# Kernel tuning notes

Hardware: AMD Instinct MI355X
Metric: run time of the kernel (lower is better)

Reference implementation:

```python
import jax, jax.numpy as jnp
import numpy as np

S, B, E, H, O, WL, PL, T = 128, 64, 1024, 1024, 135, 64, 32, 100


def setup_inputs() -> dict:
    key = jax.random.key(0)
    ks = jax.random.split(key, 12)
    rn = lambda k, shape, s=1.0: jax.random.normal(k, shape, jnp.float32) * s
    return dict(
        encoder_states=rn(ks[0], (S, B, E)),
        encoder_hidden=rn(ks[1], (2, B, E // 2)),
        previous_poses=rn(ks[2], (PL, B, O)),
        words=rn(ks[3], (WL, B, 200)),
        real_poses_len=T,
        W_ed=rn(ks[4], (H, E), 0.02), b_ed=jnp.zeros((H,), jnp.float32),
        W_att=rn(ks[5], (H, E), 0.02), b_att=jnp.zeros((H,), jnp.float32),
        W_watt=rn(ks[6], (H, 200), 0.02), b_watt=jnp.zeros((H,), jnp.float32),
        W_ih=rn(ks[7], (3 * H, O), 0.02), W_hh=rn(ks[8], (3 * H, H), 0.02),
        b_ih=jnp.zeros((3 * H,), jnp.float32), b_hh=jnp.zeros((3 * H,), jnp.float32),
        W_out=rn(ks[9], (O, 3 * H), 0.02), b_out=jnp.zeros((O,), jnp.float32),
    )


def _gru_step(x, h, W_ih, W_hh, b_ih, b_hh):
    # PyTorch GRU cell: gates ordered (r, z, n)
    gi = x @ W_ih.T + b_ih  # [B, 3H]
    gh = h @ W_hh.T + b_hh  # [B, 3H]
    Hd = h.shape[-1]
    ir, iz, inn = gi[:, :Hd], gi[:, Hd:2 * Hd], gi[:, 2 * Hd:]
    hr, hz, hn = gh[:, :Hd], gh[:, Hd:2 * Hd], gh[:, 2 * Hd:]
    r = jax.nn.sigmoid(ir + hr)
    z = jax.nn.sigmoid(iz + hz)
    n = jnp.tanh(inn + r * hn)
    return (1.0 - z) * n + z * h


def _attend(proj, h):
    # proj: [S, B, H] (already enc_to_dec-projected), h: [B, H]
    scores = jnp.einsum('sbh,bh->bs', proj, h)
    w = jax.nn.softmax(scores, axis=1)
    return jnp.einsum('sbh,bs->bh', proj, w)  # [B, H]


def reference(encoder_states, encoder_hidden, previous_poses, words, real_poses_len,
              W_ed, b_ed, W_att, b_att, W_watt, b_watt,
              W_ih, W_hh, b_ih, b_hh, W_out, b_out):
    s, b, e = encoder_states.shape
    # take last bidirectional layer, merge directions -> [B, E]
    eh = encoder_hidden.reshape(-1, 2, b, e // 2)[-1]          # [2, B, E/2]
    h = jnp.transpose(eh, (1, 0, 2)).reshape(b, e) @ W_ed.T + b_ed  # [B, H]

    # warm-up GRU pass over previous poses (only final hidden is used)
    def warm(hc, x):
        return _gru_step(x, hc, W_ih, W_hh, b_ih, b_hh), None
    h, _ = jax.lax.scan(warm, h, previous_poses)

    # attention projections are step-invariant: hoist out of the loop
    enc_proj = encoder_states @ W_att.T + b_att   # [S, B, H]
    word_proj = words @ W_watt.T + b_watt         # [WL, B, H]

    start = previous_poses[-1]                    # [B, O]

    def step(carry, _):
        pose, hc = carry
        hc = _gru_step(pose, hc, W_ih, W_hh, b_ih, b_hh)
        ctx = _attend(enc_proj, hc)
        wctx = _attend(word_proj, hc)
        cat = jnp.concatenate([hc, ctx, wctx], axis=1)  # [B, 3H]; dropout = identity (eval)
        pose = cat @ W_out.T + b_out                    # [B, O]
        return (pose, hc), pose

    _, poses = jax.lax.scan(step, (start, h), None, length=real_poses_len)
    return poses  # [T, B, O]
```

## Files before the change

### kernel.cpp

```cpp
#include <hip/hip_runtime.h>
#include <cstdint>
#include <cstddef>

typedef unsigned short ushort_t;
typedef __attribute__((ext_vector_type(8))) short short8;
typedef __attribute__((ext_vector_type(4))) float floatx4;

#define SS 128
#define BB 64
#define EE 1024
#define HH 1024
#define OO 135
#define WLW 64
#define PLP 32
#define TT 100
#define KP 160
#define NWG 64
#define NTH 1024

#define WHH_PITCH 1032
#define WIH_PITCH 168
#define LDS_WHH   0
#define LDS_WIH   99072
#define LDS_CX    115200
#define LDS_SC    127488
#define LDS_WTS   128256
#define LDS_RED   115200
#define RED_GATE  304
#define RED_BT    1216
#define RED_REG   4864

#define FB_DTYPE 0
#define FB_FLAGS 32

static __device__ __forceinline__ float bf2f(ushort_t u) {
    union { unsigned int i; float f; } v; v.i = ((unsigned int)u) << 16; return v.f;
}
static __device__ __forceinline__ ushort_t f2bf(float f) {
    union { float f; unsigned int i; } v; v.f = f;
    unsigned int x = v.i;
    x += 0x7fffu + ((x >> 16) & 1u);
    return (ushort_t)(x >> 16);
}
static __device__ __forceinline__ float ldf(const void* p, long i, unsigned isbf) {
    if (isbf) return bf2f(((const ushort_t*)p)[i]);
    return ((const float*)p)[i];
}
static __device__ __forceinline__ short8 ldfrag(const ushort_t* p) {
    return *reinterpret_cast<const short8*>(p);
}
static __device__ __forceinline__ short8 ldfrag_l(const short* p) {
    return *reinterpret_cast<const short8*>(p);
}
static __device__ __forceinline__ int cxp(int m) {
    return ((m & 15) << 6) | (m >> 4);
}
static __device__ __forceinline__ unsigned long long sysld_u64(const void* p) {
    return __hip_atomic_load((const unsigned long long*)p, __ATOMIC_RELAXED, __HIP_MEMORY_SCOPE_SYSTEM);
}
static __device__ __forceinline__ void sysst_u16(ushort_t* p, ushort_t v) {
    __hip_atomic_store(p, v, __ATOMIC_RELAXED, __HIP_MEMORY_SCOPE_SYSTEM);
}
static __device__ __forceinline__ void sysst_u32(unsigned* p, unsigned v) {
    __hip_atomic_store(p, v, __ATOMIC_RELAXED, __HIP_MEMORY_SCOPE_SYSTEM);
}
static __device__ __forceinline__ unsigned sysld_u32(const unsigned* p) {
    return __hip_atomic_load(p, __ATOMIC_RELAXED, __HIP_MEMORY_SCOPE_SYSTEM);
}
static __device__ __forceinline__ short8 sysld_frag16(const ushort_t* p) {
    union { unsigned long long u[2]; short8 s; } r;
    r.u[0] = sysld_u64(p);
    r.u[1] = sysld_u64(p + 4);
    return r.s;
}
static __device__ __forceinline__ short8 frag_ld(const void* p, unsigned isbf,
                                                 long rowoff, int kbase, int kcap) {
    if (kbase >= kcap) {
        short8 z = {0, 0, 0, 0, 0, 0, 0, 0};
        return z;
    }
    if (isbf) return ldfrag((const ushort_t*)p + rowoff + kbase);
    const float* f = (const float*)p + rowoff + kbase;
    short8 a;
    #pragma unroll
    for (int i = 0; i < 8; ++i) a[i] = (short)f2bf(f[i]);
    return a;
}
static __device__ __forceinline__ floatx4 mfma(short8 a, short8 b, floatx4 c) {
    return __builtin_amdgcn_mfma_f32_16x16x32_bf16(a, b, c, 0, 0, 0);
}
static __device__ __forceinline__ float sigmoidf(float x) {
    x = fminf(fmaxf(x, -30.f), 30.f);
    return 1.f / (1.f + __expf(-x));
}
static __device__ __forceinline__ float tanh_f(float x) {
    x = fminf(fmaxf(x, -15.f), 15.f);
    float e = __expf(2.f * x);
    return (e - 1.f) / (e + 1.f);
}

static __device__ __forceinline__ void gbar(unsigned* flags, unsigned phase) {
    __syncthreads();
    if (threadIdx.x < 64) {
        __builtin_amdgcn_fence(__ATOMIC_RELEASE, "workgroup");
        if (threadIdx.x == 0)
            sysst_u32(&flags[(size_t)blockIdx.x * 32], phase);
        for (;;) {
            unsigned v = sysld_u32(&flags[(size_t)threadIdx.x * 32]);
            if (__all((int)(v >= phase))) break;
            __builtin_amdgcn_s_sleep(1);
        }
        __builtin_amdgcn_fence(__ATOMIC_ACQUIRE, "workgroup");
    }
    __syncthreads();
}

__global__ void k_detect(const unsigned* __restrict__ enc, unsigned* __restrict__ flag)
{
    __shared__ int cnt;
    if (threadIdx.x == 0) cnt = 0;
    __syncthreads();
    unsigned w = enc[threadIdx.x];
    unsigned ef = (w >> 7) & 0xFFu;
    if (ef >= 0x70u && ef <= 0x81u) atomicAdd(&cnt, 1);
    for (int i = threadIdx.x; i < NWG * 32; i += 256)
        sysst_u32(&flag[FB_FLAGS + i], 0u);
    __syncthreads();
    if (threadIdx.x == 0)
        flag[FB_DTYPE] = (cnt >= 200) ? 1u : 0u;
}

__global__ void k_prep(const void* __restrict__ eh, const void* __restrict__ Wih,
                       const void* __restrict__ Wout, const void* __restrict__ pp,
                       const void* __restrict__ Whh,
                       ushort_t* __restrict__ ehcat, ushort_t* __restrict__ wih_p,
                       ushort_t* __restrict__ wout_p, ushort_t* __restrict__ pp_pad,
                       ushort_t* __restrict__ pose_pad, ushort_t* __restrict__ whh_bf,
                       const unsigned* __restrict__ flag)
{
    unsigned isbf = flag[FB_DTYPE];
    long idx = (long)blockIdx.x * 256 + threadIdx.x;
    const long n1 = BB * EE;
    const long n2 = (long)3 * HH * KP;
    const long n3f = (long)144 * 3 * HH;
    const long n4 = (long)PLP * BB * KP;
    const long n5 = (long)BB * KP;
    const long n6 = (long)3 * HH * HH;
    if (idx < n1) {
        int b = (int)(idx >> 10), r = (int)(idx & 1023);
        int c = r >> 9, jj = r & 511;
        ehcat[idx] = f2bf(ldf(eh, (long)(c * BB + b) * 512 + jj, isbf));
        return;
    }
    idx -= n1;
    if (idx < n2) {
        long row = idx / KP, k = idx % KP;
        wih_p[idx] = (k < OO) ? f2bf(ldf(Wih, row * OO + k, isbf)) : (ushort_t)0; return;
    }
    idx -= n2;
    if (idx < n3f) {
        long row = idx / (3 * HH), k = idx % (3 * HH);
        wout_p[idx] = (row < OO) ? f2bf(ldf(Wout, row * (3 * HH) + k, isbf)) : (ushort_t)0; return;
    }
    idx -= n3f;
    if (idx < n4) {
        long t = idx / (BB * KP); long rem = idx % (BB * KP);
        long b = rem / KP, k = rem % KP;
        pp_pad[idx] = (k < OO) ? f2bf(ldf(pp, (t * BB + b) * OO + k, isbf)) : (ushort_t)0; return;
    }
    idx -= n4;
    if (idx < n5) { pose_pad[idx] = 0; return; }
    idx -= n5;
    if (idx < n6) { whh_bf[idx] = f2bf(ldf(Whh, idx, isbf)); return; }
}

__global__ void __launch_bounds__(256) k_gemm(
    const void* __restrict__ A, int a_bf16, int lda, int kcapA,
    const void* __restrict__ B, int b_bf16, int ldb, int kcapB,
    const void* __restrict__ biasRaw,
    float* __restrict__ outF, ushort_t* __restrict__ outB16,
    ushort_t* __restrict__ outHi, ushort_t* __restrict__ outLo,
    int ldo, int M, int N, int K, const unsigned* __restrict__ flag)
{
    unsigned isbf = flag[FB_DTYPE];
    unsigned a_isbf = a_bf16 ? 1u : isbf;
    unsigned b_isbf = b_bf16 ? 1u : isbf;
    int lane = threadIdx.x & 63;
    int wid = (blockIdx.x << 2) + (threadIdx.x >> 6);
    int ng = N >> 6;
    int mt = wid / ng, g = wid % ng;
    if (mt * 16 >= M) return;
    int col = lane & 15, quad = lane >> 4;
    long arow = (long)(mt * 16 + col) * lda;
    long brow0 = (long)((g << 6) + col) * ldb;
    long brow1 = brow0 + (long)16 * ldb;
    long brow2 = brow0 + (long)32 * ldb;
    long brow3 = brow0 + (long)48 * ldb;
    int kb = quad * 8;
    floatx4 ac0 = {0.f, 0.f, 0.f, 0.f}, ac1 = ac0, ac2 = ac0, ac3 = ac0;
    for (int k = 0; k < K; k += 32) {
        short8 av = frag_ld(A, a_isbf, arow, kb + k, kcapA);
        ac0 = mfma(av, frag_ld(B, b_isbf, brow0, kb + k, kcapB), ac0);
        ac1 = mfma(av, frag_ld(B, b_isbf, brow1, kb + k, kcapB), ac1);
        ac2 = mfma(av, frag_ld(B, b_isbf, brow2, kb + k, kcapB), ac2);
        ac3 = mfma(av, frag_ld(B, b_isbf, brow3, kb + k, kcapB), ac3);
    }
    int m0 = mt * 16 + quad * 4;
    #pragma unroll
    for (int tIdx = 0; tIdx < 4; ++tIdx) {
        floatx4 ac = (tIdx == 0) ? ac0 : (tIdx == 1) ? ac1 : (tIdx == 2) ? ac2 : ac3;
        int n = (g << 6) + tIdx * 16 + col;
        float bv = biasRaw ? ldf(biasRaw, n, isbf) : 0.f;
        #pragma unroll
        for (int r = 0; r < 4; ++r) {
            float v = ac[r] + bv;
            size_t o = (size_t)(m0 + r) * ldo + n;
            if (outF) outF[o] = v;
            if (outB16) outB16[o] = f2bf(v);
            if (outHi) {
                ushort_t hi = f2bf(v);
                outHi[o] = hi;
                outLo[o] = f2bf(v - bf2f(hi));
            }
        }
    }
}

__global__ void __launch_bounds__(1024, 4) k_persist(
    const ushort_t* __restrict__ encP,
    const ushort_t* __restrict__ wordP,
    const ushort_t* __restrict__ whh_bf, const ushort_t* __restrict__ wih_p,
    const void* __restrict__ b_ih, const void* __restrict__ b_hh,
    const ushort_t* __restrict__ wout_p,
    const void* __restrict__ b_out,
    const ushort_t* __restrict__ pp_pad, ushort_t* __restrict__ pose_pad,
    float* hFa, float* hFb, ushort_t* hhia, ushort_t* hhib,
    ushort_t* hloa, ushort_t* hlob,
    void* __restrict__ out, unsigned* flagbar)
{
    extern __shared__ char smem[];
    short* whh_lds = (short*)(smem + LDS_WHH);
    short* wih_lds = (short*)(smem + LDS_WIH);
    float* cx  = (float*)(smem + LDS_CX);
    float* sc  = (float*)(smem + LDS_SC);
    float* wts = (float*)(smem + LDS_WTS);
    float* red = (float*)(smem + LDS_RED);

    const int tid = threadIdx.x;
    const int lane = tid & 63, wv = tid >> 6;
    const int wg = blockIdx.x;
    const int col = lane & 15, quad = lane >> 4;
    const int bt = wv & 3;
    const int ks = wv >> 2;
    unsigned isbf = flagbar[FB_DTYPE];
    unsigned* flags = flagbar + FB_FLAGS;
    unsigned bphase = 0;

    float* hFs = hFa; float* hFd = hFb;
    ushort_t* hhis = hhia; ushort_t* hhid = hhib;
    ushort_t* hlos = hloa; ushort_t* hlod = hlob;

    for (int s = tid; s < 48 * 128; s += NTH) {
        int r = s >> 7;
        int ko = (s & 127) << 3;
        int g = r >> 4, rr = r & 15;
        *(short8*)(whh_lds + r * WHH_PITCH + ko) =
            ldfrag(whh_bf + (size_t)g * HH * HH + (size_t)(wg * 16 + rr) * HH + ko);
    }
    for (int s = tid; s < 48 * 20; s += NTH) {
        int r = s / 20;
        int ko = (s % 20) << 3;
        int g = r >> 4, rr = r & 15;
        *(short8*)(wih_lds + r * WIH_PITCH + ko) =
            ldfrag(wih_p + (size_t)g * HH * KP + (size_t)(wg * 16 + rr) * KP + ko);
    }
    __syncthreads();

    const int j = wg * 16 + col;
    const float bir = ldf(b_ih, j, isbf)          + ldf(b_hh, j, isbf);
    const float biz = ldf(b_ih, HH + j, isbf)     + ldf(b_hh, HH + j, isbf);
    const float bin = ldf(b_ih, 2 * HH + j, isbf);
    const float bhn = ldf(b_hh, 2 * HH + j, isbf);

    for (int t = 0; t < PLP + TT; ++t) {
        const bool dec = (t >= PLP);
        const bool warm_src = (t <= PLP);
        const ushort_t* poseA = (t < PLP)  ? (pp_pad + (size_t)t * BB * KP)
                              : (t == PLP) ? (pp_pad + (size_t)(PLP - 1) * BB * KP)
                                           : pose_pad;
        {
            const ushort_t* ah = hhis + (size_t)(bt * 16 + col) * HH + quad * 8;
            const ushort_t* al = hlos + (size_t)(bt * 16 + col) * HH + quad * 8;
            const short* w0 = whh_lds + (size_t)(0  + col) * WHH_PITCH + quad * 8;
            const short* w1 = whh_lds + (size_t)(16 + col) * WHH_PITCH + quad * 8;
            const short* w2 = whh_lds + (size_t)(32 + col) * WHH_PITCH + quad * 8;
            floatx4 aR = {0.f, 0.f, 0.f, 0.f}, aZ = aR, aNi = aR, aNh = aR;
            const int k0 = ks * 256, k1 = k0 + 256;
            #pragma unroll 4
            for (int k = k0; k < k1; k += 32) {
                short8 f0 = ldfrag_l(w0 + k), f1 = ldfrag_l(w1 + k), f2 = ldfrag_l(w2 + k);
                short8 xh = sysld_frag16(ah + k), xl = sysld_frag16(al + k);
                aR = mfma(xh, f0, aR);   aR = mfma(xl, f0, aR);
                aZ = mfma(xh, f1, aZ);   aZ = mfma(xl, f1, aZ);
                aNh = mfma(xh, f2, aNh); aNh = mfma(xl, f2, aNh);
            }
            const ushort_t* ap = poseA + (size_t)(bt * 16 + col) * KP + quad * 8;
            const short* c0 = wih_lds + (size_t)(0  + col) * WIH_PITCH + quad * 8;
            const short* c1 = wih_lds + (size_t)(16 + col) * WIH_PITCH + quad * 8;
            const short* c2 = wih_lds + (size_t)(32 + col) * WIH_PITCH + quad * 8;
            for (int k5 = ks; k5 < 5; k5 += 4) {
                int k = k5 * 32;
                short8 xp = warm_src ? ldfrag(ap + k) : sysld_frag16(ap + k);
                aR = mfma(xp, ldfrag_l(c0 + k), aR);
                aZ = mfma(xp, ldfrag_l(c1 + k), aZ);
                aNi = mfma(xp, ldfrag_l(c2 + k), aNi);
            }
            if (ks == 1 || ks == 3) {
                float* dst = red + (ks >> 1) * RED_REG + bt * RED_BT;
                #pragma unroll
                for (int r = 0; r < 4; ++r) {
                    int idx = (quad * 4 + r) * 19 + col;
                    dst[idx] = aR[r];                  dst[RED_GATE + idx] = aZ[r];
                    dst[2 * RED_GATE + idx] = aNh[r];  dst[3 * RED_GATE + idx] = aNi[r];
                }
            }
            __syncthreads();
            if (ks == 0 || ks == 2) {
                const float* sp = red + (ks >> 1) * RED_REG + bt * RED_BT;
                #pragma unroll
                for (int r = 0; r < 4; ++r) {
                    int idx = (quad * 4 + r) * 19 + col;
                    aR[r] += sp[idx];                  aZ[r] += sp[RED_GATE + idx];
                    aNh[r] += sp[2 * RED_GATE + idx];  aNi[r] += sp[3 * RED_GATE + idx];
                }
            }
            __syncthreads();
            if (ks == 2) {
                float* dst = red + bt * RED_BT;
                #pragma unroll
                for (int r = 0; r < 4; ++r) {
                    int idx = (quad * 4 + r) * 19 + col;
                    dst[idx] = aR[r];                  dst[RED_GATE + idx] = aZ[r];
                    dst[2 * RED_GATE + idx] = aNh[r];  dst[3 * RED_GATE + idx] = aNi[r];
                }
            }
            __syncthreads();
            if (ks == 0) {
                const float* sp = red + bt * RED_BT;
                #pragma unroll
                for (int r = 0; r < 4; ++r) {
                    int idx = (quad * 4 + r) * 19 + col;
                    aR[r] += sp[idx];                  aZ[r] += sp[RED_GATE + idx];
                    aNh[r] += sp[2 * RED_GATE + idx];  aNi[r] += sp[3 * RED_GATE + idx];
                }
                #pragma unroll
                for (int r = 0; r < 4; ++r) {
                    int b = bt * 16 + quad * 4 + r;
                    float hold = hFs[(size_t)b * HH + j];
                    float rg = sigmoidf(aR[r] + bir);
                    float zg = sigmoidf(aZ[r] + biz);
                    float ng = tanh_f(aNi[r] + bin + rg * (aNh[r] + bhn));
                    float hn = (1.f - zg) * ng + zg * hold;
                    hFd[(size_t)b * HH + j] = hn;
                    ushort_t hi = f2bf(hn);
                    sysst_u16(&hhid[(size_t)b * HH + j], hi);
                    sysst_u16(&hlod[(size_t)b * HH + j], f2bf(hn - bf2f(hi)));
                }
            }
        }
        { float* tf = hFs; hFs = hFd; hFd = tf; }
        { ushort_t* tp = hhis; hhis = hhid; hhid = tp;
          tp = hlos; hlos = hlod; hlod = tp; }
        ++bphase;
        gbar(flags, bphase);
        if (!dec) continue;

        {
            const int b = wg;
            if (tid < 256) {
                union { unsigned long long u; ushort_t e[4]; } h4, l4;
                h4.u = sysld_u64(hhis + (size_t)b * HH + tid * 4);
                l4.u = sysld_u64(hlos + (size_t)b * HH + tid * 4);
                #pragma unroll
                for (int i = 0; i < 4; ++i)
                    cx[cxp(tid * 4 + i)] = bf2f(h4.e[i]) + bf2f(l4.e[i]);
            }
            __syncthreads();
            float hreg[16];
            #pragma unroll
            for (int i = 0; i < 16; ++i) hreg[i] = cx[(i << 6) | lane];
            for (int idx = wv; idx < 192; idx += 16) {
                const ushort_t* rp = (idx < 128)
                    ? (encP + ((size_t)(idx * BB + b) << 10))
                    : (wordP + ((size_t)((idx - 128) * BB + b) << 10));
                short8 v0 = ldfrag(rp + lane * 16);
                short8 v1 = ldfrag(rp + lane * 16 + 8);
                float s = 0.f;
                #pragma unroll
                for (int i = 0; i < 8; ++i) s += bf2f((ushort_t)v0[i]) * hreg[i];
                #pragma unroll
                for (int i = 0; i < 8; ++i) s += bf2f((ushort_t)v1[i]) * hreg[8 + i];
                #pragma unroll
                for (int m = 1; m < 64; m <<= 1) s += __shfl_xor(s, m);
                if (lane == 0) sc[idx] = s;
            }
            __syncthreads();
            if (wv == 0) {
                float a = sc[lane], c = sc[lane + 64];
                float mx = fmaxf(a, c);
                #pragma unroll
                for (int m = 1; m < 64; m <<= 1) mx = fmaxf(mx, __shfl_xor(mx, m));
                float e0 = __expf(a - mx), e1 = __expf(c - mx);
                float sm = e0 + e1;
                #pragma unroll
                for (int m = 1; m < 64; m <<= 1) sm += __shfl_xor(sm, m);
                float inv = 1.f / sm;
                wts[lane] = e0 * inv; wts[lane + 64] = e1 * inv;
            } else if (wv == 1) {
                float a = sc[128 + lane];
                float mx = a;
                #pragma unroll
                for (int m = 1; m < 64; m <<= 1) mx = fmaxf(mx, __shfl_xor(mx, m));
                float e0 = __expf(a - mx);
                float sm = e0;
                #pragma unroll
                for (int m = 1; m < 64; m <<= 1) sm += __shfl_xor(sm, m);
                wts[128 + lane] = e0 / sm;
            }
            __syncthreads();
            if (tid < 256) {
                float a0 = 0.f, a1 = 0.f, a2 = 0.f, a3 = 0.f;
                const ushort_t* basep = encP + ((size_t)b << 10) + tid * 4;
                #pragma unroll 8
                for (int s = 0; s < SS; ++s) {
                    float w = wts[s];
                    union { unsigned long long u; ushort_t e[4]; } v;
                    v.u = *(const unsigned long long*)(basep + ((size_t)(s * BB) << 10));
                    a0 += w * bf2f(v.e[0]); a1 += w * bf2f(v.e[1]);
                    a2 += w * bf2f(v.e[2]); a3 += w * bf2f(v.e[3]);
                }
                cx[1024 + cxp(tid * 4 + 0)] = a0; cx[1024 + cxp(tid * 4 + 1)] = a1;
                cx[1024 + cxp(tid * 4 + 2)] = a2; cx[1024 + cxp(tid * 4 + 3)] = a3;
            } else if (tid < 512) {
                int tt = tid - 256;
                float a0 = 0.f, a1 = 0.f, a2 = 0.f, a3 = 0.f;
                const ushort_t* basep = wordP + ((size_t)b << 10) + tt * 4;
                #pragma unroll 8
                for (int s = 0; s < WLW; ++s) {
                    float w = wts[128 + s];
                    union { unsigned long long u; ushort_t e[4]; } v;
                    v.u = *(const unsigned long long*)(basep + ((size_t)(s * BB) << 10));
                    a0 += w * bf2f(v.e[0]); a1 += w * bf2f(v.e[1]);
                    a2 += w * bf2f(v.e[2]); a3 += w * bf2f(v.e[3]);
                }
                cx[2048 + cxp(tt * 4 + 0)] = a0; cx[2048 + cxp(tt * 4 + 1)] = a1;
                cx[2048 + cxp(tt * 4 + 2)] = a2; cx[2048 + cxp(tt * 4 + 3)] = a3;
            }
            __syncthreads();
            float cr[48];
            #pragma unroll
            for (int c3 = 0; c3 < 3; ++c3)
                #pragma unroll
                for (int i = 0; i < 16; ++i)
                    cr[c3 * 16 + i] = cx[c3 * 1024 + (i << 6) + lane];
            int td = t - PLP;
            for (int oo = 0; oo < 9; ++oo) {
                int o = wv * 9 + oo;
                const ushort_t* wr = wout_p + (size_t)o * (3 * HH) + lane * 16;
                float s = 0.f;
                #pragma unroll
                for (int c3 = 0; c3 < 3; ++c3) {
                    short8 w8a = ldfrag(wr + c3 * 1024);
                    short8 w8b = ldfrag(wr + c3 * 1024 + 8);
                    #pragma unroll
                    for (int i = 0; i < 8; ++i) s += bf2f((ushort_t)w8a[i]) * cr[c3 * 16 + i];
                    #pragma unroll
                    for (int i = 0; i < 8; ++i) s += bf2f((ushort_t)w8b[i]) * cr[c3 * 16 + 8 + i];
                }
                #pragma unroll
                for (int m = 1; m < 64; m <<= 1) s += __shfl_xor(s, m);
                if (lane == 0) {
                    float v = s + ((o < OO) ? ldf(b_out, o, isbf) : 0.f);
                    if (o < OO) {
                        size_t oi = ((size_t)td * BB + b) * OO + o;
                        if (isbf) ((ushort_t*)out)[oi] = f2bf(v);
                        else      ((float*)out)[oi] = v;
                    }
                    sysst_u16(&pose_pad[(size_t)b * KP + o], (o < OO) ? f2bf(v) : (ushort_t)0);
                }
            }
        }
        ++bphase;
        gbar(flags, bphase);
    }
}

extern "C" void kernel_launch(void* const* d_in, const int* in_sizes, int n_in,
                              void* d_out, int out_size, void* d_ws, size_t ws_size,
                              hipStream_t stream)
{
    (void)in_sizes; (void)n_in; (void)out_size; (void)ws_size;
    const void* enc_states = d_in[0];
    const void* enc_hidden = d_in[1];
    const void* prev_poses = d_in[2];
    const void* words      = d_in[3];
    const void* W_ed  = d_in[5];
    const void* b_ed  = d_in[6];
    const void* W_att = d_in[7];
    const void* b_att = d_in[8];
    const void* W_watt = d_in[9];
    const void* b_watt = d_in[10];
    const void* W_ih  = d_in[11];
    const void* W_hh  = d_in[12];
    const void* b_ih  = d_in[13];
    const void* b_hh  = d_in[14];
    const void* W_out = d_in[15];
    const void* b_out = d_in[16];

    char* base = (char*)d_ws;
    size_t off = 0;
    auto alloc = [&](size_t bytes) -> char* {
        char* p = base + off;
        off = (off + bytes + 255) & ~(size_t)255;
        return p;
    };
    unsigned* flagbar  = (unsigned*)alloc(128 + (size_t)NWG * 128);
    ushort_t* ehcat    = (ushort_t*)alloc((size_t)BB * EE * 2);
    ushort_t* wih_p    = (ushort_t*)alloc((size_t)3 * HH * KP * 2);
    ushort_t* wout_p   = (ushort_t*)alloc((size_t)144 * 3 * HH * 2);
    ushort_t* pp_pad   = (ushort_t*)alloc((size_t)PLP * BB * KP * 2);
    ushort_t* pose_pad = (ushort_t*)alloc((size_t)BB * KP * 2);
    ushort_t* whh_bf   = (ushort_t*)alloc((size_t)3 * HH * HH * 2);
    float*    hF0      = (float*)alloc((size_t)BB * HH * 4);
    float*    hF1      = (float*)alloc((size_t)BB * HH * 4);
    ushort_t* hhi0     = (ushort_t*)alloc((size_t)BB * HH * 2);
    ushort_t* hhi1     = (ushort_t*)alloc((size_t)BB * HH * 2);
    ushort_t* hlo0     = (ushort_t*)alloc((size_t)BB * HH * 2);
    ushort_t* hlo1     = (ushort_t*)alloc((size_t)BB * HH * 2);
    ushort_t* encP     = (ushort_t*)alloc((size_t)SS * BB * HH * 2);
    ushort_t* wordP    = (ushort_t*)alloc((size_t)WLW * BB * HH * 2);

    k_detect<<<1, 256, 0, stream>>>((const unsigned*)enc_states, flagbar);

    k_prep<<<17512, 256, 0, stream>>>(enc_hidden, W_ih, W_out, prev_poses, W_hh,
                                      ehcat, wih_p, wout_p, pp_pad, pose_pad, whh_bf,
                                      flagbar);

    k_gemm<<<16, 256, 0, stream>>>(ehcat, 1, EE, EE, W_ed, 0, EE, EE, b_ed,
                                   hF0, nullptr, hhi0, hlo0, HH, BB, HH, EE, flagbar);
    k_gemm<<<2048, 256, 0, stream>>>(enc_states, 0, EE, EE, W_att, 0, EE, EE, b_att,
                                     nullptr, encP, nullptr, nullptr, HH, SS * BB, HH, EE, flagbar);
    k_gemm<<<1024, 256, 0, stream>>>(words, 0, 200, 200, W_watt, 0, 200, 200, b_watt,
                                     nullptr, wordP, nullptr, nullptr, HH, WLW * BB, HH, 224, flagbar);

    (void)hipFuncSetAttribute((const void*)k_persist,
                              hipFuncAttributeMaxDynamicSharedMemorySize, 154112);
    k_persist<<<NWG, NTH, 154112, stream>>>(encP, wordP, whh_bf, wih_p,
                                            b_ih, b_hh, wout_p, b_out, pp_pad, pose_pad,
                                            hF0, hF1, hhi0, hhi1, hlo0, hlo1,
                                            d_out, flagbar);
}
```

Measured before the change: 6.171 ms.

## Overlap next-step recurrent matmul with grid barrier and split attention reductions

The grid barrier is split into separate arrive and wait phases. During decode steps, the next step's h·W_hh MFMA partial products run between the two phases, so they overlap with waiting on other workgroups. The four-way cross-wave gate reduction now uses LDS atomicAdd into a single buffer, which is zeroed after use, replacing the two-stage store/sync tree. The context weighted sums are spread across twice as many threads, with a partial-sum combine, and the score loop treats encP and wordP as one contiguous row array. The gains depend on h already being complete at the early call point, and on the two projection buffers being allocated back to back.

Measured after the change: 8.825 ms. 43.0% more time.

```diff
diff --git a/kernel.cpp b/kernel.cpp
--- a/kernel.cpp
+++ b/kernel.cpp
@@ -25,10 +25,11 @@
 #define LDS_CX    115200
 #define LDS_SC    127488
 #define LDS_WTS   128256
-#define LDS_RED   115200
+#define LDS_PART  129024
+#define LDS_RED   137216
 #define RED_GATE  304
 #define RED_BT    1216
-#define RED_REG   4864
+#define SMEM_SZ   156672
 
 #define FB_DTYPE 0
 #define FB_FLAGS 32
@@ -99,12 +100,15 @@
     return (e - 1.f) / (e + 1.f);
 }
 
-static __device__ __forceinline__ void gbar(unsigned* flags, unsigned phase) {
+static __device__ __forceinline__ void g_arrive(unsigned* flags, unsigned phase) {
     __syncthreads();
+    if (threadIdx.x == 0) {
+        __builtin_amdgcn_fence(__ATOMIC_RELEASE, "workgroup");
+        sysst_u32(&flags[(size_t)blockIdx.x * 32], phase);
+    }
+}
+static __device__ __forceinline__ void g_wait(unsigned* flags, unsigned phase) {
     if (threadIdx.x < 64) {
-        __builtin_amdgcn_fence(__ATOMIC_RELEASE, "workgroup");
-        if (threadIdx.x == 0)
-            sysst_u32(&flags[(size_t)blockIdx.x * 32], phase);
         for (;;) {
             unsigned v = sysld_u32(&flags[(size_t)threadIdx.x * 32]);
             if (__all((int)(v >= phase))) break;
@@ -113,6 +117,10 @@
         __builtin_amdgcn_fence(__ATOMIC_ACQUIRE, "workgroup");
     }
     __syncthreads();
+}
+static __device__ __forceinline__ void gbar(unsigned* flags, unsigned phase) {
+    g_arrive(flags, phase);
+    g_wait(flags, phase);
 }
 
 __global__ void k_detect(const unsigned* __restrict__ enc, unsigned* __restrict__ flag)
@@ -227,8 +235,8 @@
 }
 
 __global__ void __launch_bounds__(1024, 4) k_persist(
-    const ushort_t* __restrict__ encP,
-    const ushort_t* __restrict__ wordP,
+    const ushort_t* encP,
+    const ushort_t* wordP,
     const ushort_t* __restrict__ whh_bf, const ushort_t* __restrict__ wih_p,
     const void* __restrict__ b_ih, const void* __restrict__ b_hh,
     const ushort_t* __restrict__ wout_p,
@@ -241,10 +249,11 @@
     extern __shared__ char smem[];
     short* whh_lds = (short*)(smem + LDS_WHH);
     short* wih_lds = (short*)(smem + LDS_WIH);
-    float* cx  = (float*)(smem + LDS_CX);
-    float* sc  = (float*)(smem + LDS_SC);
-    float* wts = (float*)(smem + LDS_WTS);
-    float* red = (float*)(smem + LDS_RED);
+    float* cx   = (float*)(smem + LDS_CX);
+    float* sc   = (float*)(smem + LDS_SC);
+    float* wts  = (float*)(smem + LDS_WTS);
+    float* part = (float*)(smem + LDS_PART);
+    float* red  = (float*)(smem + LDS_RED);
 
     const int tid = threadIdx.x;
     const int lane = tid & 63, wv = tid >> 6;
@@ -274,6 +283,7 @@
         *(short8*)(wih_lds + r * WIH_PITCH + ko) =
             ldfrag(wih_p + (size_t)g * HH * KP + (size_t)(wg * 16 + rr) * KP + ko);
     }
+    for (int i = tid; i < 4 * RED_BT; i += NTH) red[i] = 0.f;
     __syncthreads();
 
     const int j = wg * 16 + col;
@@ -281,6 +291,29 @@
     const float biz = ldf(b_ih, HH + j, isbf)     + ldf(b_hh, HH + j, isbf);
     const float bin = ldf(b_ih, 2 * HH + j, isbf);
     const float bhn = ldf(b_hh, 2 * HH + j, isbf);
+
+    const short* w0 = whh_lds + (size_t)(0  + col) * WHH_PITCH + quad * 8;
+    const short* w1 = whh_lds + (size_t)(16 + col) * WHH_PITCH + quad * 8;
+    const short* w2 = whh_lds + (size_t)(32 + col) * WHH_PITCH + quad * 8;
+    const short* c0 = wih_lds + (size_t)(0  + col) * WIH_PITCH + quad * 8;
+    const short* c1 = wih_lds + (size_t)(16 + col) * WIH_PITCH + quad * 8;
+    const short* c2 = wih_lds + (size_t)(32 + col) * WIH_PITCH + quad * 8;
+    const int k0 = ks * 256, k1 = k0 + 256;
+
+    floatx4 pR = {0.f, 0.f, 0.f, 0.f}, pZ = pR, pNh = pR;
+
+    auto part1 = [&]() {
+        const ushort_t* ah = hhis + (size_t)(bt * 16 + col) * HH + quad * 8;
+        const ushort_t* al = hlos + (size_t)(bt * 16 + col) * HH + quad * 8;
+        #pragma unroll 4
+        for (int k = k0; k < k1; k += 32) {
+            short8 f0 = ldfrag_l(w0 + k), f1 = ldfrag_l(w1 + k), f2 = ldfrag_l(w2 + k);
+            short8 xh = sysld_frag16(ah + k), xl = sysld_frag16(al + k);
+            pR = mfma(xh, f0, pR);   pR = mfma(xl, f0, pR);
+            pZ = mfma(xh, f1, pZ);   pZ = mfma(xl, f1, pZ);
+            pNh = mfma(xh, f2, pNh); pNh = mfma(xl, f2, pNh);
+        }
+    };
 
     for (int t = 0; t < PLP + TT; ++t) {
         const bool dec = (t >= PLP);
@@ -289,25 +322,10 @@
                               : (t == PLP) ? (pp_pad + (size_t)(PLP - 1) * BB * KP)
                                            : pose_pad;
         {
-            const ushort_t* ah = hhis + (size_t)(bt * 16 + col) * HH + quad * 8;
-            const ushort_t* al = hlos + (size_t)(bt * 16 + col) * HH + quad * 8;
-            const short* w0 = whh_lds + (size_t)(0  + col) * WHH_PITCH + quad * 8;
-            const short* w1 = whh_lds + (size_t)(16 + col) * WHH_PITCH + quad * 8;
-            const short* w2 = whh_lds + (size_t)(32 + col) * WHH_PITCH + quad * 8;
-            floatx4 aR = {0.f, 0.f, 0.f, 0.f}, aZ = aR, aNi = aR, aNh = aR;
-            const int k0 = ks * 256, k1 = k0 + 256;
-            #pragma unroll 4
-            for (int k = k0; k < k1; k += 32) {
-                short8 f0 = ldfrag_l(w0 + k), f1 = ldfrag_l(w1 + k), f2 = ldfrag_l(w2 + k);
-                short8 xh = sysld_frag16(ah + k), xl = sysld_frag16(al + k);
-                aR = mfma(xh, f0, aR);   aR = mfma(xl, f0, aR);
-                aZ = mfma(xh, f1, aZ);   aZ = mfma(xl, f1, aZ);
-                aNh = mfma(xh, f2, aNh); aNh = mfma(xl, f2, aNh);
-            }
+            if (t <= PLP) part1();
+            floatx4 aR = pR, aZ = pZ, aNh = pNh, aNi = {0.f, 0.f, 0.f, 0.f};
+            pR = aNi; pZ = aNi; pNh = aNi;
             const ushort_t* ap = poseA + (size_t)(bt * 16 + col) * KP + quad * 8;
-            const short* c0 = wih_lds + (size_t)(0  + col) * WIH_PITCH + quad * 8;
-            const short* c1 = wih_lds + (size_t)(16 + col) * WIH_PITCH + quad * 8;
-            const short* c2 = wih_lds + (size_t)(32 + col) * WIH_PITCH + quad * 8;
             for (int k5 = ks; k5 < 5; k5 += 4) {
                 int k = k5 * 32;
                 short8 xp = warm_src ? ldfrag(ap + k) : sysld_frag16(ap + k);
@@ -315,43 +333,27 @@
                 aZ = mfma(xp, ldfrag_l(c1 + k), aZ);
                 aNi = mfma(xp, ldfrag_l(c2 + k), aNi);
             }
-            if (ks == 1 || ks == 3) {
-                float* dst = red + (ks >> 1) * RED_REG + bt * RED_BT;
+            if (ks != 0) {
+                float* dst = red + bt * RED_BT;
                 #pragma unroll
                 for (int r = 0; r < 4; ++r) {
                     int idx = (quad * 4 + r) * 19 + col;
-                    dst[idx] = aR[r];                  dst[RED_GATE + idx] = aZ[r];
-                    dst[2 * RED_GATE + idx] = aNh[r];  dst[3 * RED_GATE + idx] = aNi[r];
+                    atomicAdd(&dst[idx], aR[r]);
+                    atomicAdd(&dst[RED_GATE + idx], aZ[r]);
+                    atomicAdd(&dst[2 * RED_GATE + idx], aNh[r]);
+                    atomicAdd(&dst[3 * RED_GATE + idx], aNi[r]);
                 }
             }
             __syncthreads();
-            if (ks == 0 || ks == 2) {
-                const float* sp = red + (ks >> 1) * RED_REG + bt * RED_BT;
+            if (ks == 0) {
+                float* sp = red + bt * RED_BT;
                 #pragma unroll
                 for (int r = 0; r < 4; ++r) {
                     int idx = (quad * 4 + r) * 19 + col;
-                    aR[r] += sp[idx];                  aZ[r] += sp[RED_GATE + idx];
-                    aNh[r] += sp[2 * RED_GATE + idx];  aNi[r] += sp[3 * RED_GATE + idx];
-                }
-            }
-            __syncthreads();
-            if (ks == 2) {
-                float* dst = red + bt * RED_BT;
-                #pragma unroll
-                for (int r = 0; r < 4; ++r) {
-                    int idx = (quad * 4 + r) * 19 + col;
-                    dst[idx] = aR[r];                  dst[RED_GATE + idx] = aZ[r];
-                    dst[2 * RED_GATE + idx] = aNh[r];  dst[3 * RED_GATE + idx] = aNi[r];
-                }
-            }
-            __syncthreads();
-            if (ks == 0) {
-                const float* sp = red + bt * RED_BT;
-                #pragma unroll
-                for (int r = 0; r < 4; ++r) {
-                    int idx = (quad * 4 + r) * 19 + col;
-                    aR[r] += sp[idx];                  aZ[r] += sp[RED_GATE + idx];
-                    aNh[r] += sp[2 * RED_GATE + idx];  aNi[r] += sp[3 * RED_GATE + idx];
+                    aR[r] += sp[idx];                  sp[idx] = 0.f;
+                    aZ[r] += sp[RED_GATE + idx];       sp[RED_GATE + idx] = 0.f;
+                    aNh[r] += sp[2 * RED_GATE + idx];  sp[2 * RED_GATE + idx] = 0.f;
+                    aNi[r] += sp[3 * RED_GATE + idx];  sp[3 * RED_GATE + idx] = 0.f;
                 }
                 #pragma unroll
                 for (int r = 0; r < 4; ++r) {
@@ -389,10 +391,10 @@
             float hreg[16];
             #pragma unroll
             for (int i = 0; i < 16; ++i) hreg[i] = cx[(i << 6) | lane];
+            const ushort_t* rows = encP;
+            #pragma unroll 4
             for (int idx = wv; idx < 192; idx += 16) {
-                const ushort_t* rp = (idx < 128)
-                    ? (encP + ((size_t)(idx * BB + b) << 10))
-                    : (wordP + ((size_t)((idx - 128) * BB + b) << 10));
+                const ushort_t* rp = rows + ((size_t)(idx * BB + b) << 10);
                 short8 v0 = ldfrag(rp + lane * 16);
                 short8 v1 = ldfrag(rp + lane * 16 + 8);
                 float s = 0.f;
@@ -428,33 +430,59 @@
                 wts[128 + lane] = e0 / sm;
             }
             __syncthreads();
-            if (tid < 256) {
+            if (tid < 512) {
+                int tt = tid & 255, sg = tid >> 8;
                 float a0 = 0.f, a1 = 0.f, a2 = 0.f, a3 = 0.f;
-                const ushort_t* basep = encP + ((size_t)b << 10) + tid * 4;
+                const ushort_t* basep = encP + ((size_t)b << 10) + tt * 4
+                                        + (((size_t)(sg * 64 * BB)) << 10);
+                const float* wp = wts + sg * 64;
                 #pragma unroll 8
-                for (int s = 0; s < SS; ++s) {
-                    float w = wts[s];
+                for (int s = 0; s < 64; ++s) {
+                    float w = wp[s];
                     union { unsigned long long u; ushort_t e[4]; } v;
                     v.u = *(const unsigned long long*)(basep + ((size_t)(s * BB) << 10));
                     a0 += w * bf2f(v.e[0]); a1 += w * bf2f(v.e[1]);
                     a2 += w * bf2f(v.e[2]); a3 += w * bf2f(v.e[3]);
                 }
-                cx[1024 + cxp(tid * 4 + 0)] = a0; cx[1024 + cxp(tid * 4 + 1)] = a1;
-                cx[1024 + cxp(tid * 4 + 2)] = a2; cx[1024 + cxp(tid * 4 + 3)] = a3;
-            } else if (tid < 512) {
-                int tt = tid - 256;
+                if (sg == 0) {
+                    cx[1024 + cxp(tt * 4 + 0)] = a0; cx[1024 + cxp(tt * 4 + 1)] = a1;
+                    cx[1024 + cxp(tt * 4 + 2)] = a2; cx[1024 + cxp(tt * 4 + 3)] = a3;
+                } else {
+                    part[cxp(tt * 4 + 0)] = a0; part[cxp(tt * 4 + 1)] = a1;
+                    part[cxp(tt * 4 + 2)] = a2; part[cxp(tt * 4 + 3)] = a3;
+                }
+            } else {
+                int tt = tid & 255, sg = (tid >> 8) - 2;
                 float a0 = 0.f, a1 = 0.f, a2 = 0.f, a3 = 0.f;
-                const ushort_t* basep = wordP + ((size_t)b << 10) + tt * 4;
+                const ushort_t* basep = wordP + ((size_t)b << 10) + tt * 4
+                                        + (((size_t)(sg * 32 * BB)) << 10);
+                const float* wp = wts + 128 + sg * 32;
                 #pragma unroll 8
-                for (int s = 0; s < WLW; ++s) {
-                    float w = wts[128 + s];
+                for (int s = 0; s < 32; ++s) {
+                    float w = wp[s];
                     union { unsigned long long u; ushort_t e[4]; } v;
                     v.u = *(const unsigned long long*)(basep + ((size_t)(s * BB) << 10));
                     a0 += w * bf2f(v.e[0]); a1 += w * bf2f(v.e[1]);
                     a2 += w * bf2f(v.e[2]); a3 += w * bf2f(v.e[3]);
                 }
-                cx[2048 + cxp(tt * 4 + 0)] = a0; cx[2048 + cxp(tt * 4 + 1)] = a1;
-                cx[2048 + cxp(tt * 4 + 2)] = a2; cx[2048 + cxp(tt * 4 + 3)] = a3;
+                if (sg == 0) {
+                    cx[2048 + cxp(tt * 4 + 0)] = a0; cx[2048 + cxp(tt * 4 + 1)] = a1;
+                    cx[2048 + cxp(tt * 4 + 2)] = a2; cx[2048 + cxp(tt * 4 + 3)] = a3;
+                } else {
+                    part[1024 + cxp(tt * 4 + 0)] = a0; part[1024 + cxp(tt * 4 + 1)] = a1;
+                    part[1024 + cxp(tt * 4 + 2)] = a2; part[1024 + cxp(tt * 4 + 3)] = a3;
+                }
+            }
+            __syncthreads();
+            if (tid < 256) {
+                #pragma unroll
+                for (int i = 0; i < 4; ++i)
+                    cx[1024 + cxp(tid * 4 + i)] += part[cxp(tid * 4 + i)];
+            } else if (tid < 512) {
+                int tt = tid - 256;
+                #pragma unroll
+                for (int i = 0; i < 4; ++i)
+                    cx[2048 + cxp(tt * 4 + i)] += part[1024 + cxp(tt * 4 + i)];
             }
             __syncthreads();
             float cr[48];
@@ -464,6 +492,7 @@
                 for (int i = 0; i < 16; ++i)
                     cr[c3 * 16 + i] = cx[c3 * 1024 + (i << 6) + lane];
             int td = t - PLP;
+            #pragma unroll 3
             for (int oo = 0; oo < 9; ++oo) {
                 int o = wv * 9 + oo;
                 const ushort_t* wr = wout_p + (size_t)o * (3 * HH) + lane * 16;
@@ -491,7 +520,9 @@
             }
         }
         ++bphase;
-        gbar(flags, bphase);
+        g_arrive(flags, bphase);
+        if (t + 1 < PLP + TT) part1();
+        g_wait(flags, bphase);
     }
 }
 
@@ -554,9 +585,9 @@
                                      nullptr, wordP, nullptr, nullptr, HH, WLW * BB, HH, 224, flagbar);
 
     (void)hipFuncSetAttribute((const void*)k_persist,
-                              hipFuncAttributeMaxDynamicSharedMemorySize, 154112);
-    k_persist<<<NWG, NTH, 154112, stream>>>(encP, wordP, whh_bf, wih_p,
-                                            b_ih, b_hh, wout_p, b_out, pp_pad, pose_pad,
-                                            hF0, hF1, hhi0, hhi1, hlo0, hlo1,
-                                            d_out, flagbar);
-}
+                              hipFuncAttributeMaxDynamicSharedMemorySize, SMEM_SZ);
+    k_persist<<<NWG, NTH, SMEM_SZ, stream>>>(encP, wordP, whh_bf, wih_p,
+                                             b_ih, b_hh, wout_p, b_out, pp_pad, pose_pad,
+                                             hF0, hF1, hhi0, hhi1, hlo0, hlo1,
+                                             d_out, flagbar);
+}
```
